# Performance work log

Measured on AMD Instinct MI355X. Metric: run time of the kernel, lower is better.

Reference implementation:

```python
import jax, jax.numpy as jnp
import numpy as np

B, Q, K = 4, 256, 1024          # batch, query_len, key_len
DQ, DK, DV, H = 512, 512, 512, 256  # query/key/value dims, num_hiddens


def setup_inputs() -> dict:
    key = jax.random.key(0)
    ks = jax.random.split(key, 7)
    return {
        "queries": jax.random.normal(ks[0], (B, Q, DQ), jnp.float32),
        "keys": jax.random.normal(ks[1], (B, K, DK), jnp.float32),
        "values": jax.random.normal(ks[2], (B, K, DV), jnp.float32),
        "valid_lens": jax.random.randint(ks[3], (B,), 1, K + 1),
        "Wq": jax.random.normal(ks[4], (H, DQ), jnp.float32) / np.sqrt(DQ).astype(np.float32),
        "Wk": jax.random.normal(ks[5], (H, DK), jnp.float32) / np.sqrt(DK).astype(np.float32),
        "wv": jax.random.normal(ks[6], (H,), jnp.float32) / np.sqrt(H).astype(np.float32),
    }


def reference(queries, keys, values, valid_lens, Wq, Wk, wv):
    # Linear projections (bias=False), torch Linear weight layout (out, in)
    q = jnp.einsum("bqd,hd->bqh", queries, Wq)          # (B, Q, H)
    k = jnp.einsum("bkd,hd->bkh", keys, Wk)             # (B, K, H)
    # Broadcast add -> tanh -> scalar score per (q, k) pair
    feats = jnp.tanh(q[:, :, None, :] + k[:, None, :, :])  # (B, Q, K, H)
    scores = jnp.einsum("bqkh,h->bqk", feats, wv)           # (B, Q, K)
    # masked_softmax with 1D valid_lens: mask applies along key axis per batch
    kv_len = scores.shape[-1]
    mask = jnp.arange(kv_len)[None, None, :] < valid_lens[:, None, None]  # (B,1,K)
    scores = jnp.where(mask, scores, jnp.float32(-1e6))
    attn = jax.nn.softmax(scores, axis=-1)               # (B, Q, K)
    # dropout is identity in eval mode
    return jnp.einsum("bqk,bkv->bqv", attn, values)      # (B, Q, DV)
```

## Files before the change

kernel.cpp:

```cpp
#include <hip/hip_runtime.h>
#include <stdint.h>


#define NB 4
#define NQ 256
#define NK 1024
#define ND 512
#define NH 256
#define QROWS 4
#define PJR 16
#define PJH 64

#define C2L2E 2.8853900817779268f
#define L2E   1.4426950408889634f

typedef float v2f __attribute__((ext_vector_type(2)));

__device__ void ff_vldec(const int* p, int* v) {
  bool ok = true;
  for (int i = 0; i < 4; ++i) { int x = p[i]; if (x < 1 || x > NK) ok = false; }
  if (ok) { for (int i = 0; i < 4; ++i) v[i] = p[i]; return; }
  ok = true;
  for (int i = 0; i < 4; ++i) {
    if (p[2 * i + 1] != 0) ok = false;
    int x = p[2 * i]; if (x < 1 || x > NK) ok = false;
  }
  if (ok) { for (int i = 0; i < 4; ++i) v[i] = p[2 * i]; return; }
  ok = true;
  for (int i = 0; i < 4; ++i) {
    union { int i; float f; } u; u.i = p[i];
    if (!(u.f >= 1.0f && u.f <= 1024.0f && u.f == floorf(u.f))) ok = false;
  }
  if (ok) {
    for (int i = 0; i < 4; ++i) { union { int i; float f; } u; u.i = p[i]; v[i] = (int)u.f; }
    return;
  }
  ok = true;
  for (int i = 0; i < 4; ++i) {
    union { long long l; double d; } u;
    u.l = ((long long)p[2 * i + 1] << 32) | (unsigned int)p[2 * i];
    if (!(u.d >= 1.0 && u.d <= 1024.0 && u.d == floor(u.d))) ok = false;
  }
  if (ok) {
    for (int i = 0; i < 4; ++i) {
      union { long long l; double d; } u;
      u.l = ((long long)p[2 * i + 1] << 32) | (unsigned int)p[2 * i];
      v[i] = (int)u.d;
    }
    return;
  }
  const uint16_t* hh = (const uint16_t*)p;
  const short*    s  = (const short*)p;
  ok = true;
  for (int i = 0; i < 4; ++i) { int x = s[i]; if (x < 1 || x > NK) ok = false; }
  if (ok) { for (int i = 0; i < 4; ++i) v[i] = s[i]; return; }
  ok = true;
  for (int i = 0; i < 4; ++i) {
    union { uint16_t u; _Float16 h; } u; u.u = hh[i];
    float f = (float)u.h;
    if (!(f >= 1.0f && f <= 1024.0f && f == floorf(f))) ok = false;
  }
  if (ok) {
    for (int i = 0; i < 4; ++i) {
      union { uint16_t u; _Float16 h; } u; u.u = hh[i];
      v[i] = (int)(float)u.h;
    }
    return;
  }
  ok = true;
  for (int i = 0; i < 4; ++i) {
    union { uint32_t u; float f; } u; u.u = ((uint32_t)hh[i]) << 16;
    if (!(u.f >= 1.0f && u.f <= 1028.0f)) ok = false;
  }
  if (ok) {
    for (int i = 0; i < 4; ++i) {
      union { uint32_t u; float f; } u; u.u = ((uint32_t)hh[i]) << 16;
      int x = (int)(u.f + 0.5f); if (x > NK) x = NK; v[i] = x;
    }
    return;
  }
  for (int i = 0; i < 4; ++i) v[i] = NK;
}

__global__ __launch_bounds__(256) void ff_wt(
    const float* __restrict__ Wq, const float* __restrict__ Wk,
    float* __restrict__ WTq, float* __restrict__ WTk)
{
  const int idx = blockIdx.x * 256 + threadIdx.x;
  const int d4 = idx & 127, h = idx >> 7;
  const float* src = blockIdx.y ? Wk : Wq;
  float*       dst = blockIdx.y ? WTk : WTq;
  float4 w = *(const float4*)(src + (size_t)h * ND + d4 * 4);
  w.x *= C2L2E; w.y *= C2L2E; w.z *= C2L2E; w.w *= C2L2E;
  *(float4*)(dst + ((size_t)d4 * NH + h) * 4) = w;
}

__global__ __launch_bounds__(256) void ff_proj(
    const float* __restrict__ q_in, const float* __restrict__ k_in,
    const float* __restrict__ WTq, const float* __restrict__ WTk,
    float* __restrict__ qp, float* __restrict__ kp)
{
  __shared__ float xs[PJR * ND];
  const int t  = threadIdx.x;
  const int rg = blockIdx.x >> 2;
  const int h0 = (blockIdx.x & 3) * PJH;
  const int gr0 = rg * PJR;
  const bool isq = gr0 < NB * NQ;
  const float* xin = isq ? (q_in + (size_t)gr0 * ND)
                         : (k_in + (size_t)(gr0 - NB * NQ) * ND);
  const float4* wt4 = (const float4*)(isq ? WTq : WTk);

  #pragma unroll
  for (int i = 0; i < 8; ++i)
    ((float4*)xs)[t + 256 * i] = ((const float4*)xin)[t + 256 * i];
  __syncthreads();

  const int L  = t & 63;
  const int rw = t >> 6;
  float a0 = 0.f, a1 = 0.f, a2 = 0.f, a3 = 0.f;
  const float4* xr = (const float4*)xs + (size_t)(4 * rw) * 128;

  #pragma unroll 4
  for (int d4 = 0; d4 < ND / 4; ++d4) {
    float4 w  = wt4[(size_t)d4 * NH + h0 + L];
    float4 x0 = xr[d4];
    float4 x1 = xr[128 + d4];
    float4 x2 = xr[256 + d4];
    float4 x3 = xr[384 + d4];
    a0 += w.x*x0.x + w.y*x0.y + w.z*x0.z + w.w*x0.w;
    a1 += w.x*x1.x + w.y*x1.y + w.z*x1.z + w.w*x1.w;
    a2 += w.x*x2.x + w.y*x2.y + w.z*x2.z + w.w*x2.w;
    a3 += w.x*x3.x + w.y*x3.y + w.z*x3.z + w.w*x3.w;
  }
  a0 = __builtin_amdgcn_exp2f(a0);
  a1 = __builtin_amdgcn_exp2f(a1);
  a2 = __builtin_amdgcn_exp2f(a2);
  a3 = __builtin_amdgcn_exp2f(a3);

  if (isq) {
    const int h = h0 + L;
    float* o = qp + (size_t)(gr0 + 4 * rw) * NH + h;
    o[0] = a0; o[NH] = a1; o[2 * NH] = a2; o[3 * NH] = a3;
  } else {
    __syncthreads();
    float* trs = xs;
    *(float4*)&trs[L * 16 + 4 * rw] = make_float4(a0, a1, a2, a3);
    __syncthreads();
    const int kl = t & 15, jl = t >> 4;
    const int g0 = gr0 - NB * NQ;
    const int bb = g0 >> 10, kg0 = g0 & (NK - 1);
    const int j0 = (blockIdx.x & 3) * 16;
    float4 o4 = make_float4(trs[(4*jl+0)*16 + kl], trs[(4*jl+1)*16 + kl],
                            trs[(4*jl+2)*16 + kl], trs[(4*jl+3)*16 + kl]);
    ((float4*)kp)[((size_t)bb * 64 + j0 + jl) * 1024 + kg0 + kl] = o4;
  }
}

__global__ __launch_bounds__(1024) void ff_attn_s(
    const float* __restrict__ qp, const float* __restrict__ kp,
    const int* __restrict__ vlraw, const float* __restrict__ wvp,
    float* __restrict__ Eg, float* __restrict__ Sg)
{
  __shared__ float  qs[QROWS * NH];
  __shared__ float4 wspp[NH / 2];
  __shared__ float  pstp[2 * NK * 5];
  __shared__ float  psum[16 * 4];

  const int t  = threadIdx.x;
  const int q4 = blockIdx.x;
  const int b  = blockIdx.y;

  qs[t] = qp[((size_t)b * NQ + q4 * QROWS) * NH + t];
  if (t < NH / 2) {
    float w0 = wvp[2 * t], w1 = wvp[2 * t + 1];
    wspp[t] = make_float4(-2.0f * w0, -2.0f * w1, -2.0f * (w0 + w1), 0.0f);
  }
  __syncthreads();

  int vls[4];
  ff_vldec(vlraw, vls);
  const int vl = vls[b];

  const int kk = t & 255, rh = (t >> 8) & 1, hs = t >> 9;
  const int k0 = kk * 4;

  v2f acc0 = {0.f,0.f}, acc1 = {0.f,0.f}, acc2 = {0.f,0.f}, acc3 = {0.f,0.f};
  {
    const float4* kvp = (const float4*)kp + (size_t)b * 64 * 1024 + k0;
    const float* q0p = qs + (2 * rh) * NH;
    const float* q1p = qs + (2 * rh + 1) * NH;

    #pragma unroll 2
    for (int jj = 0; jj < 32; ++jj) {
      const int j = hs * 32 + jj;
      const float4* kj = kvp + ((size_t)j << 10);
      float4 K0 = kj[0], K1 = kj[1], K2 = kj[2], K3 = kj[3];
      float4 A0 = *(const float4*)(q0p + 4 * j);
      float4 A1 = *(const float4*)(q1p + 4 * j);
      float4 wa = wspp[2 * j];
      float4 wb = wspp[2 * j + 1];
      v2f one; one.x = 1.0f; one.y = 1.0f;

#define FF_PAIRK(K4, ACC)                                                  \
      {                                                                    \
        v2f a, b2, D, N, w0v, w1v, rD;                                     \
        a.x  = A0.x * K4.x; a.y  = A1.x * K4.x;                            \
        b2.x = A0.y * K4.y; b2.y = A1.y * K4.y;                            \
        D = (one + a) * (one + b2);                                        \
        N.x = wa.z; N.y = wa.z;                                            \
        w0v.x = wa.x; w0v.y = wa.x;                                        \
        w1v.x = wa.y; w1v.y = wa.y;                                        \
        N += w0v * b2; N += w1v * a;                                       \
        rD.x = __builtin_amdgcn_rcpf(D.x);                                 \
        rD.y = __builtin_amdgcn_rcpf(D.y);                                 \
        ACC += N * rD;                                                     \
        a.x  = A0.z * K4.z; a.y  = A1.z * K4.z;                            \
        b2.x = A0.w * K4.w; b2.y = A1.w * K4.w;                            \
        D = (one + a) * (one + b2);                                        \
        N.x = wb.z; N.y = wb.z;                                            \
        w0v.x = wb.x; w0v.y = wb.x;                                        \
        w1v.x = wb.y; w1v.y = wb.y;                                        \
        N += w0v * b2; N += w1v * a;                                       \
        rD.x = __builtin_amdgcn_rcpf(D.x);                                 \
        rD.y = __builtin_amdgcn_rcpf(D.y);                                 \
        ACC += N * rD;                                                     \
      }
      FF_PAIRK(K0, acc0)
      FF_PAIRK(K1, acc1)
      FF_PAIRK(K2, acc2)
      FF_PAIRK(K3, acc3)
#undef FF_PAIRK
    }
  }

  {
    float* p = &pstp[(size_t)(hs * NK + k0) * 5 + 2 * rh];
    p[0] = acc0.x; p[1] = acc0.y;
    p[5] = acc1.x; p[6] = acc1.y;
    p[10] = acc2.x; p[11] = acc2.y;
    p[15] = acc3.x; p[16] = acc3.y;
  }
  __syncthreads();

  {
    const int k = t;
    const float* p0 = &pstp[(size_t)k * 5];
    const float* p1 = &pstp[(size_t)(NK + k) * 5];
    const bool okm = k < vl;
    float e0 = okm ? __builtin_amdgcn_exp2f((p0[0] + p1[0]) * L2E) : 0.f;
    float e1 = okm ? __builtin_amdgcn_exp2f((p0[1] + p1[1]) * L2E) : 0.f;
    float e2 = okm ? __builtin_amdgcn_exp2f((p0[2] + p1[2]) * L2E) : 0.f;
    float e3 = okm ? __builtin_amdgcn_exp2f((p0[3] + p1[3]) * L2E) : 0.f;
    ((float4*)Eg)[((size_t)b * 64 + q4) * NK + k] = make_float4(e0, e1, e2, e3);
    float s0 = e0, s1 = e1, s2 = e2, s3 = e3;
    for (int o = 32; o; o >>= 1) {
      s0 += __shfl_xor(s0, o); s1 += __shfl_xor(s1, o);
      s2 += __shfl_xor(s2, o); s3 += __shfl_xor(s3, o);
    }
    if ((t & 63) == 0)
      *(float4*)&psum[(t >> 6) * 4] = make_float4(s0, s1, s2, s3);
  }
  __syncthreads();
  if (t < 4) {
    float S = 0.f;
    #pragma unroll
    for (int w = 0; w < 16; ++w) S += psum[w * 4 + t];
    Sg[(((size_t)b * 64 + q4)) * 4 + t] = S;
  }
}

__global__ __launch_bounds__(256) void ff_pv(
    const float* __restrict__ vals, const float* __restrict__ Eg,
    const float* __restrict__ Sg, const int* __restrict__ vlraw,
    float* __restrict__ out)
{
  __shared__ float part[8 * 4 * 64];
  const int t  = threadIdx.x;
  const int ct = blockIdx.x;
  const int q4 = blockIdx.y;
  const int b  = blockIdx.z;

  int vls[4];
  ff_vldec(vlraw, vls);
  const int vl = vls[b];

  const int cl = t & 31, kq = t >> 5;
  const int c  = ct * 64 + cl * 2;
  const int k0 = kq * 128;
  int klen = vl - k0; klen = klen < 0 ? 0 : (klen > 128 ? 128 : klen);

  const float*  vb = vals + (size_t)b * NK * ND + (size_t)k0 * ND + c;
  const float4* ep = (const float4*)Eg + ((size_t)b * 64 + q4) * NK + k0;

  v2f a0 = {0.f,0.f}, a1 = {0.f,0.f}, a2 = {0.f,0.f}, a3 = {0.f,0.f};
  #pragma unroll 4
  for (int k = 0; k < klen; ++k) {
    float4 E = ep[k];
    v2f v = *(const v2f*)(vb + (size_t)k * ND);
    v2f e;
    e.x = E.x; e.y = E.x; a0 += e * v;
    e.x = E.y; e.y = E.y; a1 += e * v;
    e.x = E.z; e.y = E.z; a2 += e * v;
    e.x = E.w; e.y = E.w; a3 += e * v;
  }
  {
    float* pp = &part[(size_t)(kq * 4) * 64 + cl * 2];
    *(v2f*)(pp      ) = a0;
    *(v2f*)(pp + 64 ) = a1;
    *(v2f*)(pp + 128) = a2;
    *(v2f*)(pp + 192) = a3;
  }
  __syncthreads();
  {
    const int r = t >> 6, cc = t & 63;
    float s = 0.f;
    #pragma unroll
    for (int q = 0; q < 8; ++q) s += part[(size_t)(q * 4 + r) * 64 + cc];
    const float S = Sg[(((size_t)b * 64 + q4)) * 4 + r];
    out[((size_t)b * NQ + q4 * QROWS + r) * ND + ct * 64 + cc] = s / S;
  }
}

__global__ __launch_bounds__(1024) void ff_attn(
    const float* __restrict__ qp, const float* __restrict__ kp,
    const float* __restrict__ vals, const int* __restrict__ vlraw,
    const float* __restrict__ wvp, float* __restrict__ out)
{
  __shared__ float qs[QROWS * NH];
  __shared__ float ws[NH];
  __shared__ float st[NK * QROWS];
  __shared__ float pm[16], psm[16];
  __shared__ float part[4 * QROWS * ND];

  const int t  = threadIdx.x;
  const int q0 = blockIdx.x * QROWS;
  const int b  = blockIdx.y;

  {
    const float* qsrc = qp + ((size_t)b * NQ + q0) * NH;
    qs[t] = qsrc[t];
    if (t < NH) ws[t] = -2.0f * wvp[t];
  }
  __syncthreads();

  int vls[4];
  ff_vldec(vlraw, vls);
  const int vl = vls[b];

  float sc[4] = {0.f, 0.f, 0.f, 0.f};
  {
    const float4* kvp = (const float4*)kp + ((size_t)b * 64) * 1024 + t;
    for (int j = 0; j < 64; ++j) {
      float4 K4 = kvp[(size_t)j << 10];
      const float* wj = &ws[4 * j];
      #pragma unroll
      for (int r = 0; r < 4; ++r) {
        const float* qr = &qs[r * NH + 4 * j];
        sc[r] += wj[0] * __builtin_amdgcn_rcpf(1.0f + qr[0] * K4.x);
        sc[r] += wj[1] * __builtin_amdgcn_rcpf(1.0f + qr[1] * K4.y);
        sc[r] += wj[2] * __builtin_amdgcn_rcpf(1.0f + qr[2] * K4.z);
        sc[r] += wj[3] * __builtin_amdgcn_rcpf(1.0f + qr[3] * K4.w);
      }
    }
  }
  {
    const bool okm = (t < vl);
    *(float4*)&st[t * 4] = make_float4(okm ? sc[0] : -1e6f, okm ? sc[1] : -1e6f,
                                       okm ? sc[2] : -1e6f, okm ? sc[3] : -1e6f);
  }
  __syncthreads();

  {
    const int wid = t >> 6, lane = t & 63;
    const int row = wid >> 2, seg = wid & 3;
    const int kb = seg * 256 + lane;
    float v0 = st[(kb      ) * 4 + row];
    float v1 = st[(kb +  64) * 4 + row];
    float v2 = st[(kb + 128) * 4 + row];
    float v3 = st[(kb + 192) * 4 + row];
    float m = fmaxf(fmaxf(v0, v1), fmaxf(v2, v3));
    for (int o = 32; o; o >>= 1) m = fmaxf(m, __shfl_xor(m, o));
    if (lane == 0) pm[wid] = m;
    __syncthreads();
    m = fmaxf(fmaxf(pm[row*4+0], pm[row*4+1]), fmaxf(pm[row*4+2], pm[row*4+3]));
    float e0 = __builtin_amdgcn_exp2f((v0 - m) * L2E);
    float e1 = __builtin_amdgcn_exp2f((v1 - m) * L2E);
    float e2 = __builtin_amdgcn_exp2f((v2 - m) * L2E);
    float e3 = __builtin_amdgcn_exp2f((v3 - m) * L2E);
    float sm = e0 + e1 + e2 + e3;
    for (int o = 32; o; o >>= 1) sm += __shfl_xor(sm, o);
    if (lane == 0) psm[wid] = sm;
    __syncthreads();
    const float S = psm[row*4+0] + psm[row*4+1] + psm[row*4+2] + psm[row*4+3];
    const float rr = 1.0f / S;
    st[(kb      ) * 4 + row] = e0 * rr;
    st[(kb +  64) * 4 + row] = e1 * rr;
    st[(kb + 128) * 4 + row] = e2 * rr;
    st[(kb + 192) * 4 + row] = e3 * rr;
  }
  __syncthreads();

  {
    const int kq = t >> 8, c2 = (t & 255) * 2;
    const float* vb = vals + (size_t)b * NK * ND + c2;
    v2f o0 = {0.f,0.f}, o1 = {0.f,0.f}, o2 = {0.f,0.f}, o3 = {0.f,0.f};
    const int k0 = kq * 256;
    #pragma unroll 8
    for (int k = k0; k < k0 + 256; ++k) {
      v2f vv = *(const v2f*)(vb + (size_t)k * ND);
      float4 a = *(const float4*)&st[k * 4];
      v2f ax; ax.x = a.x; ax.y = a.x;
      v2f ay; ay.x = a.y; ay.y = a.y;
      v2f az; az.x = a.z; az.y = a.z;
      v2f aw; aw.x = a.w; aw.y = a.w;
      o0 += ax * vv; o1 += ay * vv; o2 += az * vv; o3 += aw * vv;
    }
    float* pp = &part[(size_t)kq * QROWS * ND + c2];
    *(v2f*)(pp         ) = o0;
    *(v2f*)(pp +     ND) = o1;
    *(v2f*)(pp + 2 * ND) = o2;
    *(v2f*)(pp + 3 * ND) = o3;
  }
  __syncthreads();
  {
    const int r = t >> 8, c2 = (t & 255) * 2;
    const float* pp = &part[(size_t)r * ND + c2];
    v2f s = {0.f, 0.f};
    #pragma unroll
    for (int kq = 0; kq < 4; ++kq) s += *(const v2f*)(pp + (size_t)kq * QROWS * ND);
    *(v2f*)(out + ((size_t)b * NQ + q0 + r) * ND + c2) = s;
  }
}

extern "C" void kernel_launch(void* const* d_in, const int* in_sizes, int n_in,
                              void* d_out, int out_size, void* d_ws, size_t ws_size,
                              hipStream_t stream) {
  const float* queries = (const float*)d_in[0];
  const float* keys    = (const float*)d_in[1];
  const float* values  = (const float*)d_in[2];
  const int*   vlens   = (const int*)d_in[3];
  const float* Wq      = (const float*)d_in[4];
  const float* Wk      = (const float*)d_in[5];
  const float* wv      = (const float*)d_in[6];
  float* out = (float*)d_out;

  float* qp  = (float*)d_ws;
  float* kp  = qp  + (size_t)NB * NQ * NH;
  float* wtq = kp  + (size_t)NB * NH * NK;
  float* wtk = wtq + (size_t)(ND / 4) * NH * 4;
  float* Eg  = wtk + (size_t)(ND / 4) * NH * 4;
  float* Sg  = Eg  + (size_t)NB * 64 * NK * 4;
  const size_t need = ((size_t)(Sg - (float*)d_ws) + NB * 64 * 4) * sizeof(float);

  ff_wt  <<<dim3(128, 2), 256, 0, stream>>>(Wq, Wk, wtq, wtk);
  ff_proj<<<dim3((NB * (NQ + NK) / PJR) * (NH / PJH)), 256, 0, stream>>>(
      queries, keys, wtq, wtk, qp, kp);
  if (ws_size >= need) {
    ff_attn_s<<<dim3(NQ / QROWS, NB), 1024, 0, stream>>>(
        qp, kp, vlens, wv, Eg, Sg);
    ff_pv<<<dim3(8, NQ / QROWS, NB), 256, 0, stream>>>(
        values, Eg, Sg, vlens, out);
  } else {
    ff_attn<<<dim3(NQ / QROWS, NB), 1024, 0, stream>>>(
        qp, kp, values, vlens, wv, out);
  }
}
```

Before: 177.1 us.

## Split score kernel over key halves and reduce hidden partials with shuffles

The score kernel now launches twice as many blocks, each covering half of the key axis. Each thread handles a quarter of the hidden dimension instead of half, and the four hidden partials are combined with cross-lane shuffles instead of a large shared-memory staging buffer. Each block writes a partial softmax denominator per key half, and the PV kernel adds the two halves. This increases parallelism, halves shared memory use and removes one barrier, and the launch bounds hint for higher occupancy. The cost is extra shuffles, more blocks each reloading the queries, and a slightly larger workspace.

```diff
diff --git a/kernel.cpp b/kernel.cpp
--- a/kernel.cpp
+++ b/kernel.cpp
@@ -156,19 +156,20 @@
   }
 }
 
-__global__ __launch_bounds__(1024) void ff_attn_s(
+__global__ __launch_bounds__(1024, 8) void ff_attn_s(
     const float* __restrict__ qp, const float* __restrict__ kp,
     const int* __restrict__ vlraw, const float* __restrict__ wvp,
     float* __restrict__ Eg, float* __restrict__ Sg)
 {
   __shared__ float  qs[QROWS * NH];
   __shared__ float4 wspp[NH / 2];
-  __shared__ float  pstp[2 * NK * 5];
-  __shared__ float  psum[16 * 4];
+  __shared__ float  el[512 * 4];
+  __shared__ float  psum[32];
 
   const int t  = threadIdx.x;
-  const int q4 = blockIdx.x;
-  const int b  = blockIdx.y;
+  const int kh = blockIdx.x;
+  const int q4 = blockIdx.y;
+  const int b  = blockIdx.z;
 
   qs[t] = qp[((size_t)b * NQ + q4 * QROWS) * NH + t];
   if (t < NH / 2) {
@@ -181,8 +182,11 @@
   ff_vldec(vlraw, vls);
   const int vl = vls[b];
 
-  const int kk = t & 255, rh = (t >> 8) & 1, hs = t >> 9;
-  const int k0 = kk * 4;
+  const int l  = t & 63, w = t >> 6;
+  const int hs = l >> 4, kl = l & 15;
+  const int kw = w & 7,  rh = w >> 3;
+  const int kk = kw * 16 + kl;
+  const int k0 = kh * 512 + kk * 4;
 
   v2f acc0 = {0.f,0.f}, acc1 = {0.f,0.f}, acc2 = {0.f,0.f}, acc3 = {0.f,0.f};
   {
@@ -190,9 +194,8 @@
     const float* q0p = qs + (2 * rh) * NH;
     const float* q1p = qs + (2 * rh + 1) * NH;
 
-    #pragma unroll 2
-    for (int jj = 0; jj < 32; ++jj) {
-      const int j = hs * 32 + jj;
+    for (int jj = 0; jj < 16; ++jj) {
+      const int j = hs * 16 + jj;
       const float4* kj = kvp + ((size_t)j << 10);
       float4 K0 = kj[0], K1 = kj[1], K2 = kj[2], K3 = kj[3];
       float4 A0 = *(const float4*)(q0p + 4 * j);
@@ -233,39 +236,51 @@
     }
   }
 
-  {
-    float* p = &pstp[(size_t)(hs * NK + k0) * 5 + 2 * rh];
-    p[0] = acc0.x; p[1] = acc0.y;
-    p[5] = acc1.x; p[6] = acc1.y;
-    p[10] = acc2.x; p[11] = acc2.y;
-    p[15] = acc3.x; p[16] = acc3.y;
-  }
-  __syncthreads();
-
-  {
-    const int k = t;
-    const float* p0 = &pstp[(size_t)k * 5];
-    const float* p1 = &pstp[(size_t)(NK + k) * 5];
-    const bool okm = k < vl;
-    float e0 = okm ? __builtin_amdgcn_exp2f((p0[0] + p1[0]) * L2E) : 0.f;
-    float e1 = okm ? __builtin_amdgcn_exp2f((p0[1] + p1[1]) * L2E) : 0.f;
-    float e2 = okm ? __builtin_amdgcn_exp2f((p0[2] + p1[2]) * L2E) : 0.f;
-    float e3 = okm ? __builtin_amdgcn_exp2f((p0[3] + p1[3]) * L2E) : 0.f;
-    ((float4*)Eg)[((size_t)b * 64 + q4) * NK + k] = make_float4(e0, e1, e2, e3);
-    float s0 = e0, s1 = e1, s2 = e2, s3 = e3;
-    for (int o = 32; o; o >>= 1) {
-      s0 += __shfl_xor(s0, o); s1 += __shfl_xor(s1, o);
-      s2 += __shfl_xor(s2, o); s3 += __shfl_xor(s3, o);
-    }
-    if ((t & 63) == 0)
-      *(float4*)&psum[(t >> 6) * 4] = make_float4(s0, s1, s2, s3);
-  }
-  __syncthreads();
+#define FF_RED(v)                                                          \
+  v.x += __shfl_xor(v.x, 16); v.x += __shfl_xor(v.x, 32);                  \
+  v.y += __shfl_xor(v.y, 16); v.y += __shfl_xor(v.y, 32);
+  FF_RED(acc0) FF_RED(acc1) FF_RED(acc2) FF_RED(acc3)
+#undef FF_RED
+
+  float ex0, ey0, ex1, ey1, ex2, ey2, ex3, ey3;
+  {
+    const bool m0 = (k0 + 0) < vl, m1 = (k0 + 1) < vl;
+    const bool m2 = (k0 + 2) < vl, m3 = (k0 + 3) < vl;
+    ex0 = m0 ? __builtin_amdgcn_exp2f(acc0.x * L2E) : 0.f;
+    ey0 = m0 ? __builtin_amdgcn_exp2f(acc0.y * L2E) : 0.f;
+    ex1 = m1 ? __builtin_amdgcn_exp2f(acc1.x * L2E) : 0.f;
+    ey1 = m1 ? __builtin_amdgcn_exp2f(acc1.y * L2E) : 0.f;
+    ex2 = m2 ? __builtin_amdgcn_exp2f(acc2.x * L2E) : 0.f;
+    ey2 = m2 ? __builtin_amdgcn_exp2f(acc2.y * L2E) : 0.f;
+    ex3 = m3 ? __builtin_amdgcn_exp2f(acc3.x * L2E) : 0.f;
+    ey3 = m3 ? __builtin_amdgcn_exp2f(acc3.y * L2E) : 0.f;
+  }
+
+  if (hs == 0) {
+    const int klc = kk * 4;
+    el[(klc + 0) * 4 + 2 * rh] = ex0; el[(klc + 0) * 4 + 2 * rh + 1] = ey0;
+    el[(klc + 1) * 4 + 2 * rh] = ex1; el[(klc + 1) * 4 + 2 * rh + 1] = ey1;
+    el[(klc + 2) * 4 + 2 * rh] = ex2; el[(klc + 2) * 4 + 2 * rh + 1] = ey2;
+    el[(klc + 3) * 4 + 2 * rh] = ex3; el[(klc + 3) * 4 + 2 * rh + 1] = ey3;
+  }
+  {
+    float sl = (hs == 0) ? ((ex0 + ex1) + (ex2 + ex3)) : 0.f;
+    float sh = (hs == 0) ? ((ey0 + ey1) + (ey2 + ey3)) : 0.f;
+    for (int o = 32; o; o >>= 1) { sl += __shfl_xor(sl, o); sh += __shfl_xor(sh, o); }
+    if (l == 0) { psum[w * 2] = sl; psum[w * 2 + 1] = sh; }
+  }
+  __syncthreads();
+
+  if (t < 512)
+    ((float4*)Eg)[((size_t)b * 64 + q4) * NK + kh * 512 + t]
+        = *(const float4*)&el[t * 4];
+
   if (t < 4) {
+    const int c = t & 1, base = (t >> 1) * 8;
     float S = 0.f;
     #pragma unroll
-    for (int w = 0; w < 16; ++w) S += psum[w * 4 + t];
-    Sg[(((size_t)b * 64 + q4)) * 4 + t] = S;
+    for (int kw2 = 0; kw2 < 8; ++kw2) S += psum[(base + kw2) * 2 + c];
+    Sg[(((size_t)b * 64 + q4) * 4 + t) * 2 + kh] = S;
   }
 }
 
@@ -316,7 +331,8 @@
     float s = 0.f;
     #pragma unroll
     for (int q = 0; q < 8; ++q) s += part[(size_t)(q * 4 + r) * 64 + cc];
-    const float S = Sg[(((size_t)b * 64 + q4)) * 4 + r];
+    const size_t sb = ((size_t)b * 64 + q4) * 4 + r;
+    const float S = Sg[sb * 2] + Sg[sb * 2 + 1];
     out[((size_t)b * NQ + q4 * QROWS + r) * ND + ct * 64 + cc] = s / S;
   }
 }
@@ -450,13 +466,13 @@
   float* wtk = wtq + (size_t)(ND / 4) * NH * 4;
   float* Eg  = wtk + (size_t)(ND / 4) * NH * 4;
   float* Sg  = Eg  + (size_t)NB * 64 * NK * 4;
-  const size_t need = ((size_t)(Sg - (float*)d_ws) + NB * 64 * 4) * sizeof(float);
+  const size_t need = ((size_t)(Sg - (float*)d_ws) + NB * 64 * 4 * 2) * sizeof(float);
 
   ff_wt  <<<dim3(128, 2), 256, 0, stream>>>(Wq, Wk, wtq, wtk);
   ff_proj<<<dim3((NB * (NQ + NK) / PJR) * (NH / PJH)), 256, 0, stream>>>(
       queries, keys, wtq, wtk, qp, kp);
   if (ws_size >= need) {
-    ff_attn_s<<<dim3(NQ / QROWS, NB), 1024, 0, stream>>>(
+    ff_attn_s<<<dim3(2, NQ / QROWS, NB), 1024, 0, stream>>>(
         qp, kp, vlens, wv, Eg, Sg);
     ff_pv<<<dim3(8, NQ / QROWS, NB), 256, 0, stream>>>(
         values, Eg, Sg, vlens, out);
```

Result: no change. 174.7 us (-1.3%).
